# Kernel tuning notes

Measured on AMD Instinct MI355X. Metric: run time of the kernel, lower is better.

Reference implementation:

```python
import jax, jax.numpy as jnp
import numpy as np

N_NODES = 100000
N_EDGES = 1600000
D_IN = 128
D_OUT = 128


def setup_inputs() -> dict:
    key = jax.random.key(0)
    k1, k2, k3, k4, k5, k6 = jax.random.split(key, 6)
    x = jax.random.normal(k1, (N_NODES, D_IN), dtype=jnp.float32)
    edge_src = jax.random.randint(k2, (N_EDGES,), 0, N_NODES, dtype=jnp.int64 if jax.config.jax_enable_x64 else jnp.int32)
    edge_dst = jax.random.randint(k3, (N_EDGES,), 0, N_NODES, dtype=jnp.int64 if jax.config.jax_enable_x64 else jnp.int32)
    edge_val = jax.random.uniform(k4, (N_EDGES,), dtype=jnp.float32)
    # nn.Linear(2*D_IN, D_OUT): store W as [2*D_IN, D_OUT] (transposed torch layout)
    W = jax.random.normal(k5, (2 * D_IN, D_OUT), dtype=jnp.float32) * (1.0 / np.sqrt(2 * D_IN))
    b = jax.random.normal(k6, (D_OUT,), dtype=jnp.float32) * 0.01
    return {"x": x, "edge_src": edge_src, "edge_dst": edge_dst, "edge_val": edge_val, "W": W, "b": b}


def reference(x, edge_src, edge_dst, edge_val, W, b):
    # support = adj @ x  (sparse COO: adj[dst, src] = edge_val)
    gathered = x[edge_src] * edge_val[:, None]               # [E, D_IN]
    support = jax.ops.segment_sum(gathered, edge_dst, num_segments=x.shape[0])  # [N, D_IN]
    # concat self + aggregated neighbor features, then linear
    h = jnp.concatenate([x, support], axis=1)                # [N, 2*D_IN]
    return h @ W + b                                          # [N, D_OUT]
```

## Files before the change

kernel.cpp:

```cpp
#include <hip/hip_runtime.h>

#define D 128
#define BN 64
#define NBIN 391
#define NBMAX 512
#define CHUNK 2048
#define SCAP 12

typedef __attribute__((ext_vector_type(8))) short bf16x8;
typedef __attribute__((ext_vector_type(4))) float f32x4;

__device__ __forceinline__ unsigned short f2bf(float f) {
    unsigned int u = __builtin_bit_cast(unsigned int, f);
    u = (u + 0x7fffu + ((u >> 16) & 1u)) >> 16;
    return (unsigned short)u;
}
__device__ __forceinline__ float bf2f(unsigned int u) {
    return __builtin_bit_cast(float, u << 16);
}

__global__ void prep_kernel(const float* __restrict__ x,
                            unsigned short* __restrict__ x_bf,
                            const float* __restrict__ W,
                            unsigned short* __restrict__ WT,
                            int* __restrict__ ccnt,
                            int n4, int XB, int WB) {
    int blk = blockIdx.x, tid = threadIdx.x;
    if (blk < XB) {
        int i = blk * 256 + tid;
        if (i < n4) {
            float4 v = ((const float4*)x)[i];
            ushort4 s;
            s.x = f2bf(v.x); s.y = f2bf(v.y); s.z = f2bf(v.z); s.w = f2bf(v.w);
            ((ushort4*)x_bf)[i] = s;
        }
    } else if (blk < XB + WB) {
        int t = (blk - XB) * 256 + tid;
        if (t < 2 * D * D) {
            int col = t & 127, k = t >> 7;
            WT[col * 256 + k] = f2bf(W[k * D + col]);
        }
    } else {
        ccnt[tid] = 0;
        ccnt[tid + 256] = 0;
    }
}

__global__ __launch_bounds__(256) void chist_kernel(const int* __restrict__ edst,
                                                    int* __restrict__ ccnt, int E) {
    __shared__ int h[NBMAX];
    for (int i = threadIdx.x; i < NBMAX; i += 256) h[i] = 0;
    __syncthreads();
    int stride = gridDim.x * 256;
    for (int e = blockIdx.x * 256 + threadIdx.x; e < E; e += stride)
        atomicAdd(&h[edst[e] >> 8], 1);
    __syncthreads();
    for (int i = threadIdx.x; i < NBIN; i += 256) {
        int c = h[i];
        if (c) atomicAdd(&ccnt[i], c);
    }
}

__global__ __launch_bounds__(256) void cscan_kernel(const int* __restrict__ ccnt,
                                                    int* __restrict__ cbase,
                                                    int* __restrict__ ccur) {
    __shared__ int p[256];
    int t = threadIdx.x;
    int s0 = ccnt[2 * t], s1 = ccnt[2 * t + 1];
    int loc = s0 + s1;
    p[t] = loc;
    __syncthreads();
    for (int off = 1; off < 256; off <<= 1) {
        int v = p[t];
        int u = (t >= off) ? p[t - off] : 0;
        __syncthreads();
        p[t] = v + u;
        __syncthreads();
    }
    int ex = p[t] - loc;
    cbase[2 * t] = ex;     ccur[2 * t] = ex;
    cbase[2 * t + 1] = ex + s0; ccur[2 * t + 1] = ex + s0;
}

__global__ __launch_bounds__(256) void cfill_kernel(const int* __restrict__ esrc,
                                                    const int* __restrict__ edst,
                                                    const float* __restrict__ eval,
                                                    int* __restrict__ ccur,
                                                    int2* __restrict__ ep, int E) {
    __shared__ int lh[NBMAX];
    __shared__ int lcur[NBMAX];
    __shared__ int p[256];
    __shared__ int2 ord[CHUNK];
    __shared__ unsigned short obk[CHUNK];

    const int tid = threadIdx.x;
    const int base = blockIdx.x * CHUNK;
    const int n = min(CHUNK, E - base);

    for (int i = tid; i < NBMAX; i += 256) lh[i] = 0;
    __syncthreads();

    int esv[8]; int ebk[8];
    float evv[8];
#pragma unroll
    for (int k = 0; k < 8; ++k) {
        int li = k * 256 + tid;
        if (li < n) {
            int i = base + li;
            int dst = edst[i];
            esv[k] = esrc[i];
            evv[k] = eval[i];
            int b = dst >> 8;
            ebk[k] = b | ((dst & 255) << 16);
            atomicAdd(&lh[b], 1);
        } else ebk[k] = -1;
    }
    __syncthreads();

    int s0 = lh[2 * tid], s1 = lh[2 * tid + 1];
    int loc = s0 + s1;
    p[tid] = loc;
    __syncthreads();
    for (int off = 1; off < 256; off <<= 1) {
        int v = p[tid];
        int u = (tid >= off) ? p[tid - off] : 0;
        __syncthreads();
        p[tid] = v + u;
        __syncthreads();
    }
    int ex = p[tid] - loc;
    lcur[2 * tid] = ex;
    lcur[2 * tid + 1] = ex + s0;
    __syncthreads();

#pragma unroll
    for (int k = 0; k < 8; ++k) {
        if (ebk[k] >= 0) {
            int b = ebk[k] & 0xffff, nl = ebk[k] >> 16;
            int slot = atomicAdd(&lcur[b], 1);
            ord[slot] = make_int2((esv[k] << 8) | nl, __builtin_bit_cast(int, evv[k]));
            obk[slot] = (unsigned short)b;
        }
    }
    __syncthreads();

    for (int b = tid; b < NBIN; b += 256) {
        int c = lh[b];
        if (c) lh[b] = atomicAdd(&ccur[b], c) - (lcur[b] - c);
    }
    __syncthreads();

    for (int i = tid; i < n; i += 256) {
        int b = obk[i];
        ep[lh[b] + i] = ord[i];
    }
}

__global__ __launch_bounds__(512) void csort_kernel(int2* __restrict__ ep,
                                                    const int* __restrict__ cbase,
                                                    const int* __restrict__ ccnt,
                                                    int* __restrict__ node_start) {
    __shared__ int h[256];
    __shared__ int p[256];

    const int t = threadIdx.x;
    const int bin = blockIdx.x;
    const int cb = cbase[bin];
    const int ce = cb + ccnt[bin];

    if (t < 256) h[t] = 0;
    __syncthreads();

    int2 ev[SCAP];
#pragma unroll
    for (int k = 0; k < SCAP; ++k) {
        int idx = cb + k * 512 + t;
        if (idx < ce) {
            int2 e = ep[idx];
            ev[k] = e;
            atomicAdd(&h[e.x & 255], 1);
        } else ev[k] = make_int2(-1, 0);
    }
    __syncthreads();

    int c = 0;
    if (t < 256) { c = h[t]; p[t] = c; }
    __syncthreads();
    for (int off = 1; off < 256; off <<= 1) {
        int v = 0, u = 0;
        if (t < 256) { v = p[t]; u = (t >= off) ? p[t - off] : 0; }
        __syncthreads();
        if (t < 256) p[t] = v + u;
        __syncthreads();
    }
    if (t < 256) {
        int st = cb + p[t] - c;
        node_start[bin * 256 + t] = st;
        h[t] = st;
    }
    __syncthreads();

#pragma unroll
    for (int k = 0; k < SCAP; ++k) {
        if (ev[k].x >= 0) {
            int nl = ev[k].x & 255;
            int pos = atomicAdd(&h[nl], 1);
            ep[pos] = make_int2(ev[k].x & 0xFFFFFF3F, ev[k].y);
        }
    }
}

__global__ __launch_bounds__(256, 4) void gather_fused_kernel(
        const unsigned short* __restrict__ x_bf,
        const int* __restrict__ node_start,
        const int2* __restrict__ edge_pack,
        const unsigned short* __restrict__ WT,
        const float* __restrict__ bias,
        float* __restrict__ out, int N) {
    __shared__ unsigned short accb[BN * 136];
    __shared__ int nb[BN + 1];

    const int tid = threadIdx.x;
    const int node0 = blockIdx.x * BN;
    const int w = tid >> 6, lane = tid & 63;
    unsigned int* accw = (unsigned int*)accb;

    for (int i = tid * 8; i < BN * 136; i += 2048)
        *(uint4*)(accb + i) = make_uint4(0u, 0u, 0u, 0u);
    if (tid <= BN) nb[tid] = node_start[node0 + tid];
    __syncthreads();

    const int js = __builtin_amdgcn_readfirstlane(nb[w * 16]);
    const int je = __builtin_amdgcn_readfirstlane(nb[w * 16 + 16]);
    const unsigned short* xl = x_bf + lane * 2;

    int cur = -1;
    float ax = 0.f, ay = 0.f;
    for (int g = js; g < je; g += 16) {
        int m = je - g; if (m > 16) m = 16;
        int2 e[16];
#pragma unroll
        for (int k = 0; k < 16; ++k) {
            int idx = g + k; if (idx >= je) idx = je - 1;
            e[k] = edge_pack[idx];
        }
        unsigned int p[16];
#pragma unroll
        for (int k = 0; k < 16; ++k)
            p[k] = *(const unsigned int*)(xl + ((e[k].x >> 8) << 7));
#pragma unroll
        for (int k = 0; k < 16; ++k) {
            if (k < m) {
                int nd = e[k].x & 63;
                if (nd != cur) {
                    if (cur >= 0)
                        accw[cur * 68 + lane] =
                            (unsigned int)f2bf(ax) | ((unsigned int)f2bf(ay) << 16);
                    cur = nd; ax = 0.f; ay = 0.f;
                }
                float v = __builtin_bit_cast(float, e[k].y);
                ax += bf2f(p[k] & 0xffffu) * v;
                ay += bf2f(p[k] >> 16) * v;
            }
        }
    }
    if (cur >= 0)
        accw[cur * 68 + lane] = (unsigned int)f2bf(ax) | ((unsigned int)f2bf(ay) << 16);
    __syncthreads();

    const int quad = lane >> 4;
    const int l15  = lane & 15;
    const int colbase = w * 32;

    f32x4 acc[4][2];
#pragma unroll
    for (int rt = 0; rt < 4; ++rt) {
        acc[rt][0] = (f32x4){0.f, 0.f, 0.f, 0.f};
        acc[rt][1] = (f32x4){0.f, 0.f, 0.f, 0.f};
    }

#pragma unroll
    for (int ks = 0; ks < 8; ++ks) {
        bf16x8 wf0 = *(const bf16x8*)(WT + (size_t)(colbase + l15) * 256 + ks * 32 + quad * 8);
        bf16x8 wf1 = *(const bf16x8*)(WT + (size_t)(colbase + 16 + l15) * 256 + ks * 32 + quad * 8);
#pragma unroll
        for (int rt = 0; rt < 4; ++rt) {
            int row = rt * 16 + l15;
            bf16x8 a;
            if (ks < 4) {
                int rg = node0 + row; if (rg >= N) rg = N - 1;
                a = *(const bf16x8*)(x_bf + (size_t)rg * D + ks * 32 + quad * 8);
            } else {
                a = *(const bf16x8*)(accb + row * 136 + (ks - 4) * 32 + quad * 8);
            }
            acc[rt][0] = __builtin_amdgcn_mfma_f32_16x16x32_bf16(a, wf0, acc[rt][0], 0, 0, 0);
            acc[rt][1] = __builtin_amdgcn_mfma_f32_16x16x32_bf16(a, wf1, acc[rt][1], 0, 0, 0);
        }
    }

#pragma unroll
    for (int ct = 0; ct < 2; ++ct) {
        int col = colbase + ct * 16 + l15;
        float bv = bias[col];
#pragma unroll
        for (int rt = 0; rt < 4; ++rt) {
#pragma unroll
            for (int rg = 0; rg < 4; ++rg) {
                int row = node0 + rt * 16 + quad * 4 + rg;
                if (row < N)
                    out[(size_t)row * D + col] = acc[rt][ct][rg] + bv;
            }
        }
    }
}

extern "C" void kernel_launch(void* const* d_in, const int* in_sizes, int n_in,
                              void* d_out, int out_size, void* d_ws, size_t ws_size,
                              hipStream_t stream) {
    const float* x    = (const float*)d_in[0];
    const int*   esrc = (const int*)d_in[1];
    const int*   edst = (const int*)d_in[2];
    const float* eval = (const float*)d_in[3];
    const float* W    = (const float*)d_in[4];
    const float* bias = (const float*)d_in[5];
    float*       out  = (float*)d_out;

    const int N  = in_sizes[0] / D;
    const int E  = in_sizes[1];
    const int NG = (N + BN - 1) / BN;

    char* ws = (char*)d_ws;
    unsigned short* x_bf  = (unsigned short*)ws;
    int2*           ep    = (int2*)(ws + 25600000);
    unsigned short* WT    = (unsigned short*)(ws + 38400000);
    int*            nbg   = (int*)(ws + 38465536);
    int*            ccnt  = (int*)(ws + 38865920);
    int*            cbase = (int*)(ws + 38867968);
    int*            ccur  = (int*)(ws + 38870016);

    const int n4 = N * D / 4;
    const int XB = (n4 + 255) / 256;
    const int WB = (2 * D * D + 255) / 256;

    prep_kernel<<<XB + WB + 1, 256, 0, stream>>>(x, x_bf, W, WT, ccnt, n4, XB, WB);
    chist_kernel<<<512, 256, 0, stream>>>(edst, ccnt, E);
    cscan_kernel<<<1, 256, 0, stream>>>(ccnt, cbase, ccur);
    cfill_kernel<<<(E + CHUNK - 1) / CHUNK, 256, 0, stream>>>(esrc, edst, eval,
                                                              ccur, ep, E);
    csort_kernel<<<NBIN, 512, 0, stream>>>(ep, cbase, ccnt, nbg);
    gather_fused_kernel<<<NG, 256, 0, stream>>>(x_bf, nbg, ep, WT, bias, out, N);
    (void)ws_size; (void)n_in; (void)out_size;
}
```

Baseline: 274.5 us.

## Make coarse bin scatter deterministic with per-chunk histograms and prefix scan

Replaces the global-atomic coarse histogram and atomic cursor claiming with per-chunk histograms written to workspace, a per-bin scan across chunks, and offset lookup in the fill kernel. Chunk size doubles to 4096 with 512-thread blocks. This removes global atomics and the ccnt zeroing but adds a kernel launch and an extra histogram pass over edge_dst. The gather kernel's occupancy hint is also raised to 8 waves per SIMD, which may force register spills.

```diff
diff --git a/kernel.cpp b/kernel.cpp
--- a/kernel.cpp
+++ b/kernel.cpp
@@ -4,7 +4,7 @@
 #define BN 64
 #define NBIN 391
 #define NBMAX 512
-#define CHUNK 2048
+#define CHUNK 4096
 #define SCAP 12
 
 typedef __attribute__((ext_vector_type(8))) short bf16x8;
@@ -23,8 +23,7 @@
                             unsigned short* __restrict__ x_bf,
                             const float* __restrict__ W,
                             unsigned short* __restrict__ WT,
-                            int* __restrict__ ccnt,
-                            int n4, int XB, int WB) {
+                            int n4, int XB) {
     int blk = blockIdx.x, tid = threadIdx.x;
     if (blk < XB) {
         int i = blk * 256 + tid;
@@ -34,36 +33,56 @@
             s.x = f2bf(v.x); s.y = f2bf(v.y); s.z = f2bf(v.z); s.w = f2bf(v.w);
             ((ushort4*)x_bf)[i] = s;
         }
-    } else if (blk < XB + WB) {
+    } else {
         int t = (blk - XB) * 256 + tid;
         if (t < 2 * D * D) {
             int col = t & 127, k = t >> 7;
             WT[col * 256 + k] = f2bf(W[k * D + col]);
         }
-    } else {
-        ccnt[tid] = 0;
-        ccnt[tid + 256] = 0;
-    }
-}
-
-__global__ __launch_bounds__(256) void chist_kernel(const int* __restrict__ edst,
-                                                    int* __restrict__ ccnt, int E) {
+    }
+}
+
+__global__ __launch_bounds__(512) void hist_kernel(const int* __restrict__ edst,
+                                                   int* __restrict__ hcnt, int E) {
     __shared__ int h[NBMAX];
-    for (int i = threadIdx.x; i < NBMAX; i += 256) h[i] = 0;
-    __syncthreads();
-    int stride = gridDim.x * 256;
-    for (int e = blockIdx.x * 256 + threadIdx.x; e < E; e += stride)
-        atomicAdd(&h[edst[e] >> 8], 1);
-    __syncthreads();
-    for (int i = threadIdx.x; i < NBIN; i += 256) {
-        int c = h[i];
-        if (c) atomicAdd(&ccnt[i], c);
-    }
+    const int t = threadIdx.x, c = blockIdx.x;
+    h[t] = 0;
+    __syncthreads();
+    const int base = c * CHUNK;
+    const int n = min(CHUNK, E - base);
+#pragma unroll
+    for (int k = 0; k < 8; ++k) {
+        int li = k * 512 + t;
+        if (li < n) atomicAdd(&h[edst[base + li] >> 8], 1);
+    }
+    __syncthreads();
+    hcnt[c * NBMAX + t] = h[t];
+}
+
+__global__ __launch_bounds__(256) void binscan_kernel(const int* __restrict__ hcnt,
+                                                      int* __restrict__ cpos,
+                                                      int* __restrict__ ccnt, int NCH) {
+    const int tid = threadIdx.x;
+    const int lane = tid & 63;
+    const int b = blockIdx.x * 4 + (tid >> 6);
+    int run = 0;
+    for (int c0 = 0; c0 < NCH; c0 += 64) {
+        int c = c0 + lane;
+        int v = (c < NCH) ? hcnt[c * NBMAX + b] : 0;
+        int s = v;
+#pragma unroll
+        for (int off = 1; off < 64; off <<= 1) {
+            int u = __shfl_up(s, off, 64);
+            if (lane >= off) s += u;
+        }
+        if (c < NCH) cpos[b * NCH + c] = run + s - v;
+        run += __shfl(s, 63, 64);
+    }
+    if (lane == 0) ccnt[b] = run;
 }
 
 __global__ __launch_bounds__(256) void cscan_kernel(const int* __restrict__ ccnt,
-                                                    int* __restrict__ cbase,
-                                                    int* __restrict__ ccur) {
+                                                    int* __restrict__ cbase) {
     __shared__ int p[256];
     int t = threadIdx.x;
     int s0 = ccnt[2 * t], s1 = ccnt[2 * t + 1];
@@ -78,33 +97,35 @@
         __syncthreads();
     }
     int ex = p[t] - loc;
-    cbase[2 * t] = ex;     ccur[2 * t] = ex;
-    cbase[2 * t + 1] = ex + s0; ccur[2 * t + 1] = ex + s0;
-}
-
-__global__ __launch_bounds__(256) void cfill_kernel(const int* __restrict__ esrc,
+    cbase[2 * t] = ex;
+    cbase[2 * t + 1] = ex + s0;
+}
+
+__global__ __launch_bounds__(512) void cfill_kernel(const int* __restrict__ esrc,
                                                     const int* __restrict__ edst,
                                                     const float* __restrict__ eval,
-                                                    int* __restrict__ ccur,
-                                                    int2* __restrict__ ep, int E) {
+                                                    const int* __restrict__ cbase,
+                                                    const int* __restrict__ cpos,
+                                                    int2* __restrict__ ep, int E, int NCH) {
     __shared__ int lh[NBMAX];
     __shared__ int lcur[NBMAX];
-    __shared__ int p[256];
+    __shared__ int p[NBMAX];
     __shared__ int2 ord[CHUNK];
     __shared__ unsigned short obk[CHUNK];
 
-    const int tid = threadIdx.x;
-    const int base = blockIdx.x * CHUNK;
+    const int t = threadIdx.x;
+    const int blk = blockIdx.x;
+    const int base = blk * CHUNK;
     const int n = min(CHUNK, E - base);
 
-    for (int i = tid; i < NBMAX; i += 256) lh[i] = 0;
+    lh[t] = 0;
     __syncthreads();
 
     int esv[8]; int ebk[8];
     float evv[8];
 #pragma unroll
     for (int k = 0; k < 8; ++k) {
-        int li = k * 256 + tid;
+        int li = k * 512 + t;
         if (li < n) {
             int i = base + li;
             int dst = edst[i];
@@ -117,20 +138,17 @@
     }
     __syncthreads();
 
-    int s0 = lh[2 * tid], s1 = lh[2 * tid + 1];
-    int loc = s0 + s1;
-    p[tid] = loc;
-    __syncthreads();
-    for (int off = 1; off < 256; off <<= 1) {
-        int v = p[tid];
-        int u = (tid >= off) ? p[tid - off] : 0;
-        __syncthreads();
-        p[tid] = v + u;
-        __syncthreads();
-    }
-    int ex = p[tid] - loc;
-    lcur[2 * tid] = ex;
-    lcur[2 * tid + 1] = ex + s0;
+    int cnt = lh[t];
+    p[t] = cnt;
+    __syncthreads();
+    for (int off = 1; off < NBMAX; off <<= 1) {
+        int v = p[t];
+        int u = (t >= off) ? p[t - off] : 0;
+        __syncthreads();
+        p[t] = v + u;
+        __syncthreads();
+    }
+    lcur[t] = p[t] - cnt;
     __syncthreads();
 
 #pragma unroll
@@ -144,13 +162,13 @@
     }
     __syncthreads();
 
-    for (int b = tid; b < NBIN; b += 256) {
-        int c = lh[b];
-        if (c) lh[b] = atomicAdd(&ccur[b], c) - (lcur[b] - c);
-    }
-    __syncthreads();
-
-    for (int i = tid; i < n; i += 256) {
+    if (t < NBIN) {
+        int c2 = lh[t];
+        if (c2) lh[t] = cbase[t] + cpos[t * NCH + blk] - (lcur[t] - c2);
+    }
+    __syncthreads();
+
+    for (int i = t; i < n; i += 512) {
         int b = obk[i];
         ep[lh[b] + i] = ord[i];
     }
@@ -210,7 +228,7 @@
     }
 }
 
-__global__ __launch_bounds__(256, 4) void gather_fused_kernel(
+__global__ __launch_bounds__(256, 8) void gather_fused_kernel(
         const unsigned short* __restrict__ x_bf,
         const int* __restrict__ node_start,
         const int2* __restrict__ edge_pack,
@@ -327,26 +345,28 @@
 
     const int N  = in_sizes[0] / D;
     const int E  = in_sizes[1];
-    const int NG = (N + BN - 1) / BN;
+    const int NG  = (N + BN - 1) / BN;
+    const int NCH = (E + CHUNK - 1) / CHUNK;
 
     char* ws = (char*)d_ws;
     unsigned short* x_bf  = (unsigned short*)ws;
     int2*           ep    = (int2*)(ws + 25600000);
+    int*            hcnt  = (int*)(ws + 25600000);
     unsigned short* WT    = (unsigned short*)(ws + 38400000);
     int*            nbg   = (int*)(ws + 38465536);
     int*            ccnt  = (int*)(ws + 38865920);
     int*            cbase = (int*)(ws + 38867968);
-    int*            ccur  = (int*)(ws + 38870016);
+    int*            cpos  = (int*)(ws + 38870016);
 
     const int n4 = N * D / 4;
     const int XB = (n4 + 255) / 256;
     const int WB = (2 * D * D + 255) / 256;
 
-    prep_kernel<<<XB + WB + 1, 256, 0, stream>>>(x, x_bf, W, WT, ccnt, n4, XB, WB);
-    chist_kernel<<<512, 256, 0, stream>>>(edst, ccnt, E);
-    cscan_kernel<<<1, 256, 0, stream>>>(ccnt, cbase, ccur);
-    cfill_kernel<<<(E + CHUNK - 1) / CHUNK, 256, 0, stream>>>(esrc, edst, eval,
-                                                              ccur, ep, E);
+    prep_kernel<<<XB + WB, 256, 0, stream>>>(x, x_bf, W, WT, n4, XB);
+    hist_kernel<<<NCH, 512, 0, stream>>>(edst, hcnt, E);
+    binscan_kernel<<<128, 256, 0, stream>>>(hcnt, cpos, ccnt, NCH);
+    cscan_kernel<<<1, 256, 0, stream>>>(ccnt, cbase);
+    cfill_kernel<<<NCH, 512, 0, stream>>>(esrc, edst, eval, cbase, cpos, ep, E, NCH);
     csort_kernel<<<NBIN, 512, 0, stream>>>(ep, cbase, ccnt, nbg);
     gather_fused_kernel<<<NG, 256, 0, stream>>>(x_bf, nbg, ep, WT, bias, out, N);
     (void)ws_size; (void)n_in; (void)out_size;
```

Result: faster. 236.1 us (-14.0%).
